# Kernel tuning notes

Measured on AMD Instinct MI355X. Metric: run time of the kernel, lower is better.

The kernel has to match this reference:

```python
import jax, jax.numpy as jnp
import numpy as np

HIDDEN = 1024
HEAD_DIM = 64
N_HEADS = HIDDEN // HEAD_DIM  # 16
BATCH = 2
SEQ = 2048
ROT_DIM = HEAD_DIM // 2  # RotaryEmbedding(head_dim // 2): only first half of head dims rotated
THETA = 10000.0
SCALE_BASE = 512.0  # lucidrains xpos default
EPS = 1e-5


def setup_inputs() -> dict:
    key = jax.random.key(0)
    ks = jax.random.split(key, 8)

    def lin(k, shape, fan_in):
        b = 1.0 / np.sqrt(fan_in)
        return jax.random.uniform(k, shape, jnp.float32, -b, b)

    return {
        "x": jax.random.normal(ks[0], (BATCH, SEQ, HIDDEN), jnp.float32),
        "ln1_w": jnp.ones((HIDDEN,), jnp.float32),
        "ln1_b": jnp.zeros((HIDDEN,), jnp.float32),
        "wqkv_w": lin(ks[1], (HIDDEN, 3 * HIDDEN), HIDDEN),
        "wg_w": lin(ks[2], (HIDDEN, HIDDEN), HIDDEN),
        "wo_w": lin(ks[3], (HIDDEN, HIDDEN), HIDDEN),
        "gn_w": jnp.ones((N_HEADS,), jnp.float32),
        "gn_b": jnp.zeros((N_HEADS,), jnp.float32),
        "ln2_w": jnp.ones((HIDDEN,), jnp.float32),
        "ln2_b": jnp.zeros((HIDDEN,), jnp.float32),
        "w1_w": lin(ks[4], (HIDDEN, HIDDEN), HIDDEN),
        "w1_b": lin(ks[5], (HIDDEN,), HIDDEN),
        "w2_w": lin(ks[6], (HIDDEN, HIDDEN), HIDDEN),
        "w2_b": lin(ks[7], (HIDDEN,), HIDDEN),
    }


def _layernorm(x, w, b):
    m = jnp.mean(x, axis=-1, keepdims=True)
    v = jnp.mean(jnp.square(x - m), axis=-1, keepdims=True)
    return (x - m) * jax.lax.rsqrt(v + EPS) * w + b


def _rotate_half(x):
    # interleaved pairs: (d r) with r=2 -> (-x2, x1)
    xs = x.reshape(x.shape[:-1] + (ROT_DIM // 2, 2))
    x1, x2 = xs[..., 0], xs[..., 1]
    return jnp.stack((-x2, x1), axis=-1).reshape(x.shape)


def _xpos_rotary(q, k):
    # lucidrains RotaryEmbedding(dim=ROT_DIM, use_xpos=True).rotate_queries_and_keys
    S = q.shape[-2]
    half = jnp.arange(0, ROT_DIM, 2, dtype=jnp.float32)
    inv_freq = 1.0 / (THETA ** (half / ROT_DIM))          # [ROT_DIM/2]
    t = jnp.arange(S, dtype=jnp.float32)
    freqs = jnp.repeat(t[:, None] * inv_freq, 2, axis=-1)  # [S, ROT_DIM] interleaved
    scale_vals = (half + 0.4 * ROT_DIM) / (1.4 * ROT_DIM)  # [ROT_DIM/2]
    power = (t - S // 2) / SCALE_BASE
    scale = scale_vals[None, :] ** power[:, None]           # [S, ROT_DIM/2]
    scale = jnp.concatenate((scale, scale), axis=-1)        # [S, ROT_DIM] (cat, not interleave)
    cos, sin = jnp.cos(freqs), jnp.sin(freqs)

    def apply(x, sc):
        xl, xr = x[..., :ROT_DIM], x[..., ROT_DIM:]
        xl = xl * cos * sc + _rotate_half(xl) * sin * sc
        return jnp.concatenate((xl, xr), axis=-1)

    return apply(q, scale), apply(k, 1.0 / scale)


def _mish(x):
    return x * jnp.tanh(jax.nn.softplus(x))


def reference(x, ln1_w, ln1_b, wqkv_w, wg_w, wo_w, gn_w, gn_b,
              ln2_w, ln2_b, w1_w, w1_b, w2_w, w2_b):
    B, S, _ = x.shape
    h = _layernorm(x, ln1_w, ln1_b)

    # qkv: [B,S,3H] -> 'B S (H D) -> B H S D' with D = 3*head_dim, then chunk 3
    qkv = (h @ wqkv_w).reshape(B, S, N_HEADS, 3 * HEAD_DIM).transpose(0, 2, 1, 3)
    q, k, v = jnp.split(qkv, 3, axis=-1)  # each [B,H,S,head_dim]
    q, k = _xpos_rotary(q, k)

    # decay mask: gamma_h^(i-j) for i>=j (causal), 0 otherwise
    gamma = 1.0 - 2.0 ** (-5.0 - jnp.arange(N_HEADS, dtype=jnp.float32))
    idx = jnp.arange(S)
    nm = (idx[:, None] - idx[None, :]).astype(jnp.float32)     # [S,S]
    decay = jnp.where(nm >= 0, gamma[:, None, None] ** nm, 0.0)  # [H,S,S]

    ret = jnp.einsum('bhsd,bhtd->bhst', q, k) * decay[None]
    ret = jnp.einsum('bhst,bhtd->bhsd', ret, v)               # [B,H,S,head_dim]

    # GroupNorm(n_heads, n_heads): normalize each head over (S, head_dim)
    m = jnp.mean(ret, axis=(2, 3), keepdims=True)
    va = jnp.mean(jnp.square(ret - m), axis=(2, 3), keepdims=True)
    ret = (ret - m) * jax.lax.rsqrt(va + EPS)
    ret = ret * gn_w[None, :, None, None] + gn_b[None, :, None, None]

    y = ret.transpose(0, 2, 1, 3).reshape(B, S, HIDDEN)       # B H S D -> B S (H D)
    y = _mish(h @ wg_w) * y
    y = y @ wo_w

    y = y + x
    z = _layernorm(y, ln2_w, ln2_b)
    ffn = jax.nn.gelu(z @ w1_w + w1_b, approximate=False) @ w2_w + w2_b
    return ffn + y
```

## Files before the change

### kernel.cpp

```cpp
#include <hip/hip_runtime.h>


constexpr int S_LEN = 2048;
constexpr int HID   = 1024;
constexpr int NH    = 16;
constexpr int HD    = 64;
constexpr int BATCH = 2;
constexpr float EPS = 1e-5f;

using short8 = __attribute__((ext_vector_type(8))) short;
using f32x4  = __attribute__((ext_vector_type(4))) float;

__device__ __forceinline__ ushort bf16rne(float x) {
  unsigned u = __float_as_uint(x);
  unsigned r = (u + 0x7fffu + ((u >> 16) & 1u)) >> 16;
  return (ushort)r;
}
__device__ __forceinline__ void split2(float x, ushort& hi, ushort& lo) {
  hi = bf16rne(x);
  float hf = __uint_as_float((unsigned)hi << 16);
  lo = bf16rne(x - hf);
}

__device__ __forceinline__ void block_reduce2(float& s, float& ss) {
  #pragma unroll
  for (int o = 32; o > 0; o >>= 1) {
    s  += __shfl_down(s, o, 64);
    ss += __shfl_down(ss, o, 64);
  }
  __shared__ float ls[4], lss[4];
  const int lane = threadIdx.x & 63;
  const int w    = threadIdx.x >> 6;
  if (lane == 0) { ls[w] = s; lss[w] = ss; }
  __syncthreads();
  if (threadIdx.x == 0) {
    float a = 0.f, b2 = 0.f;
    #pragma unroll
    for (int i = 0; i < 4; ++i) { a += ls[i]; b2 += lss[i]; }
    ls[0] = a; lss[0] = b2;
  }
  __syncthreads();
  s = ls[0]; ss = lss[0];
}

__global__ __launch_bounds__(256) void ln_split_kernel(const float* __restrict__ x,
    const float* __restrict__ w, const float* __restrict__ b,
    ushort* __restrict__ oh, ushort* __restrict__ ol) {
  const int row = blockIdx.x;
  const int t   = threadIdx.x;
  const float4 v = reinterpret_cast<const float4*>(x + (size_t)row * HID)[t];
  float s  = v.x + v.y + v.z + v.w;
  float ss = v.x*v.x + v.y*v.y + v.z*v.z + v.w*v.w;
  block_reduce2(s, ss);
  const float mean = s * (1.f / HID);
  const float var  = ss * (1.f / HID) - mean * mean;
  const float rstd = rsqrtf(var + EPS);
  const float4 wv = reinterpret_cast<const float4*>(w)[t];
  const float4 bv = reinterpret_cast<const float4*>(b)[t];
  float o[4];
  o[0] = (v.x - mean) * rstd * wv.x + bv.x;
  o[1] = (v.y - mean) * rstd * wv.y + bv.y;
  o[2] = (v.z - mean) * rstd * wv.z + bv.z;
  o[3] = (v.w - mean) * rstd * wv.w + bv.w;
  ushort4 hv, lv;
  split2(o[0], hv.x, lv.x); split2(o[1], hv.y, lv.y);
  split2(o[2], hv.z, lv.z); split2(o[3], hv.w, lv.w);
  *reinterpret_cast<ushort4*>(oh + (size_t)row * HID + t * 4) = hv;
  *reinterpret_cast<ushort4*>(ol + (size_t)row * HID + t * 4) = lv;
}

__global__ __launch_bounds__(256) void wsplit_kernel(const float* __restrict__ W,
    ushort* __restrict__ Th, ushort* __restrict__ Tl, int N) {
  __shared__ float tile[32][33];
  const int k0 = blockIdx.y * 32;
  const int n0 = blockIdx.x * 32;
  const int tx = threadIdx.x & 31, ty = threadIdx.x >> 5;
  #pragma unroll
  for (int r = 0; r < 4; ++r)
    tile[ty + 8*r][tx] = W[(size_t)(k0 + ty + 8*r) * N + n0 + tx];
  __syncthreads();
  #pragma unroll
  for (int r = 0; r < 4; ++r) {
    const int n = ty + 8*r;
    const float v = tile[tx][n];
    ushort hi, lo; split2(v, hi, lo);
    Th[(size_t)(n0 + n) * 1024 + k0 + tx] = hi;
    Tl[(size_t)(n0 + n) * 1024 + k0 + tx] = lo;
  }
}

__global__ __launch_bounds__(256) void rot_tables_kernel(float* __restrict__ tcs,
    float* __restrict__ tsn, float* __restrict__ tscq, float* __restrict__ tsck) {
  const int g = blockIdx.x * 256 + threadIdx.x;
  const int m = g & 15, s = g >> 4;
  const float invf = exp2f(-((float)(2 * m) * (1.f / 32.f)) * 13.287712379549449f);
  const float ang = (float)s * invf;
  tcs[g] = cosf(ang);
  tsn[g] = sinf(ang);
  const float p  = ((float)s - 1024.f) * (1.f / 512.f);
  const float sv = (2.f * (float)m + 12.8f) * (1.f / 44.8f);
  const float l  = log2f(sv) * p;
  tscq[g] = exp2f(l);
  tsck[g] = exp2f(-l);
}

__device__ __forceinline__ float mishf(float v) {
  return v * tanhf(log1pf(expf(v)));
}
__device__ __forceinline__ float geluf(float v) {
  return 0.5f * v * (1.f + erff(v * 0.7071067811865475f));
}

template <int EPI>
__global__ __launch_bounds__(256, 2) void gemm_mfma(
    const ushort* __restrict__ Ah, const ushort* __restrict__ Al,
    const ushort* __restrict__ Bh, const ushort* __restrict__ Bl,
    const float* __restrict__ bias, const float* __restrict__ res,
    float* __restrict__ C, ushort* __restrict__ Ch, ushort* __restrict__ Cl,
    int N, int K) {
  __shared__ ushort sA[2][128 * 64];
  __shared__ ushort sB[2][128 * 64];
  const int tid  = threadIdx.x;
  const int lane = tid & 63;
  const int w    = tid >> 6;
  const int wm   = w >> 1, wn = w & 1;
  const int rowBase = blockIdx.y * 128;
  const int colBase = blockIdx.x * 128;

  f32x4 acc[4][4] = {};

  const int l8   = lane >> 3;
  const int kswz = ((lane & 7) * 16) ^ (l8 << 4);

  for (int k0 = 0; k0 < K; k0 += 64) {
    __syncthreads();
    #pragma unroll
    for (int c = 0; c < 4; ++c) {
      const int row = w * 32 + c * 8;
      const char* gah = (const char*)(Ah + (size_t)(rowBase + row + l8) * K + k0) + kswz;
      const char* gal = (const char*)(Al + (size_t)(rowBase + row + l8) * K + k0) + kswz;
      const char* gbh = (const char*)(Bh + (size_t)(colBase + row + l8) * K + k0) + kswz;
      const char* gbl = (const char*)(Bl + (size_t)(colBase + row + l8) * K + k0) + kswz;
      __builtin_amdgcn_global_load_lds((const __attribute__((address_space(1))) void*)gah,
          (__attribute__((address_space(3))) void*)((char*)sA[0] + row * 128), 16, 0, 0);
      __builtin_amdgcn_global_load_lds((const __attribute__((address_space(1))) void*)gal,
          (__attribute__((address_space(3))) void*)((char*)sA[1] + row * 128), 16, 0, 0);
      __builtin_amdgcn_global_load_lds((const __attribute__((address_space(1))) void*)gbh,
          (__attribute__((address_space(3))) void*)((char*)sB[0] + row * 128), 16, 0, 0);
      __builtin_amdgcn_global_load_lds((const __attribute__((address_space(1))) void*)gbl,
          (__attribute__((address_space(3))) void*)((char*)sB[1] + row * 128), 16, 0, 0);
    }
    __syncthreads();
    #pragma unroll
    for (int kk = 0; kk < 2; ++kk) {
      const int kb = kk * 64 + ((lane >> 4) << 4);
      short8 ah[4], al[4], bh[4], bl[4];
      #pragma unroll
      for (int i = 0; i < 4; ++i) {
        const int row = wm * 64 + i * 16 + (lane & 15);
        const int off = row * 128 + (kb ^ ((row & 7) << 4));
        ah[i] = *(const short8*)((const char*)sA[0] + off);
        al[i] = *(const short8*)((const char*)sA[1] + off);
      }
      #pragma unroll
      for (int j = 0; j < 4; ++j) {
        const int row = wn * 64 + j * 16 + (lane & 15);
        const int off = row * 128 + (kb ^ ((row & 7) << 4));
        bh[j] = *(const short8*)((const char*)sB[0] + off);
        bl[j] = *(const short8*)((const char*)sB[1] + off);
      }
      #pragma unroll
      for (int i = 0; i < 4; ++i)
        #pragma unroll
        for (int j = 0; j < 4; ++j) {
          acc[i][j] = __builtin_amdgcn_mfma_f32_16x16x32_bf16(ah[i], bh[j], acc[i][j], 0, 0, 0);
          acc[i][j] = __builtin_amdgcn_mfma_f32_16x16x32_bf16(ah[i], bl[j], acc[i][j], 0, 0, 0);
          acc[i][j] = __builtin_amdgcn_mfma_f32_16x16x32_bf16(al[i], bh[j], acc[i][j], 0, 0, 0);
        }
    }
  }

  const int cRow = rowBase + wm * 64 + ((lane >> 4) << 2);
  const int cCol = colBase + wn * 64 + (lane & 15);
  #pragma unroll
  for (int i = 0; i < 4; ++i)
    #pragma unroll
    for (int j = 0; j < 4; ++j) {
      const int gc = cCol + j * 16;
      #pragma unroll
      for (int r = 0; r < 4; ++r) {
        const int gr = cRow + i * 16 + r;
        float v = acc[i][j][r];
        if constexpr (EPI == 1) v = mishf(v);
        if constexpr (EPI == 2) v += res[(size_t)gr * N + gc];
        if constexpr (EPI == 3) v = geluf(v + bias[gc]);
        if constexpr (EPI == 4) v += bias[gc] + res[(size_t)gr * N + gc];
        if constexpr (EPI == 3) {
          ushort hi, lo; split2(v, hi, lo);
          Ch[(size_t)gr * N + gc] = hi;
          Cl[(size_t)gr * N + gc] = lo;
        } else {
          C[(size_t)gr * N + gc] = v;
        }
      }
    }
}

__global__ __launch_bounds__(256, 2) void gemm_qkv_rot(
    const ushort* __restrict__ Ah, const ushort* __restrict__ Al,
    const ushort* __restrict__ Bh, const ushort* __restrict__ Bl,
    const float* __restrict__ tcs, const float* __restrict__ tsn,
    const float* __restrict__ tscq, const float* __restrict__ tsck,
    ushort* __restrict__ qTh, ushort* __restrict__ qTl,
    ushort* __restrict__ kTh, ushort* __restrict__ kTl,
    ushort* __restrict__ vTh, ushort* __restrict__ vTl) {
  const int N = 3072, K = 1024;
  __shared__ ushort sA[2][128 * 64];
  __shared__ ushort sB[2][128 * 64];
  const int tid  = threadIdx.x;
  const int lane = tid & 63;
  const int w    = tid >> 6;
  const int wm   = w >> 1, wn = w & 1;
  const int rowBase = blockIdx.y * 128;
  const int colBase = blockIdx.x * 128;

  f32x4 acc[4][4] = {};

  const int l8   = lane >> 3;
  const int kswz = ((lane & 7) * 16) ^ (l8 << 4);

  for (int k0 = 0; k0 < K; k0 += 64) {
    __syncthreads();
    #pragma unroll
    for (int c = 0; c < 4; ++c) {
      const int row = w * 32 + c * 8;
      const char* gah = (const char*)(Ah + (size_t)(rowBase + row + l8) * K + k0) + kswz;
      const char* gal = (const char*)(Al + (size_t)(rowBase + row + l8) * K + k0) + kswz;
      const char* gbh = (const char*)(Bh + (size_t)(colBase + row + l8) * K + k0) + kswz;
      const char* gbl = (const char*)(Bl + (size_t)(colBase + row + l8) * K + k0) + kswz;
      __builtin_amdgcn_global_load_lds((const __attribute__((address_space(1))) void*)gah,
          (__attribute__((address_space(3))) void*)((char*)sA[0] + row * 128), 16, 0, 0);
      __builtin_amdgcn_global_load_lds((const __attribute__((address_space(1))) void*)gal,
          (__attribute__((address_space(3))) void*)((char*)sA[1] + row * 128), 16, 0, 0);
      __builtin_amdgcn_global_load_lds((const __attribute__((address_space(1))) void*)gbh,
          (__attribute__((address_space(3))) void*)((char*)sB[0] + row * 128), 16, 0, 0);
      __builtin_amdgcn_global_load_lds((const __attribute__((address_space(1))) void*)gbl,
          (__attribute__((address_space(3))) void*)((char*)sB[1] + row * 128), 16, 0, 0);
    }
    __syncthreads();
    #pragma unroll
    for (int kk = 0; kk < 2; ++kk) {
      const int kb = kk * 64 + ((lane >> 4) << 4);
      short8 ah[4], al[4], bh[4], bl[4];
      #pragma unroll
      for (int i = 0; i < 4; ++i) {
        const int row = wm * 64 + i * 16 + (lane & 15);
        const int off = row * 128 + (kb ^ ((row & 7) << 4));
        ah[i] = *(const short8*)((const char*)sA[0] + off);
        al[i] = *(const short8*)((const char*)sA[1] + off);
      }
      #pragma unroll
      for (int j = 0; j < 4; ++j) {
        const int row = wn * 64 + j * 16 + (lane & 15);
        const int off = row * 128 + (kb ^ ((row & 7) << 4));
        bh[j] = *(const short8*)((const char*)sB[0] + off);
        bl[j] = *(const short8*)((const char*)sB[1] + off);
      }
      #pragma unroll
      for (int i = 0; i < 4; ++i)
        #pragma unroll
        for (int j = 0; j < 4; ++j) {
          acc[i][j] = __builtin_amdgcn_mfma_f32_16x16x32_bf16(ah[i], bh[j], acc[i][j], 0, 0, 0);
          acc[i][j] = __builtin_amdgcn_mfma_f32_16x16x32_bf16(ah[i], bl[j], acc[i][j], 0, 0, 0);
          acc[i][j] = __builtin_amdgcn_mfma_f32_16x16x32_bf16(al[i], bh[j], acc[i][j], 0, 0, 0);
        }
    }
  }

  const int c0     = colBase + wn * 64;
  const int region = (c0 >> 6) % 3;
  const int hh     = c0 / 192;
  const int cRow   = rowBase + wm * 64 + ((lane >> 4) << 2);
  const int lc     = lane & 15;

  if (region == 2) {
    #pragma unroll
    for (int j = 0; j < 4; ++j) {
      const int d = 16 * j + lc;
      #pragma unroll
      for (int i = 0; i < 4; ++i) {
        const int s0g = cRow + i * 16;
        const int bb  = s0g >> 11;
        const int s0  = s0g & 2047;
        ushort4 hv, lv;
        #pragma unroll
        for (int r = 0; r < 4; ++r) {
          ushort hi, lo; split2(acc[i][j][r], hi, lo);
          ((ushort*)&hv)[r] = hi; ((ushort*)&lv)[r] = lo;
        }
        const size_t a = ((size_t)(bb * NH + hh) * HD + d) * S_LEN + s0;
        *reinterpret_cast<ushort4*>(vTh + a) = hv;
        *reinterpret_cast<ushort4*>(vTl + a) = lv;
      }
    }
  } else {
    ushort* Oh = (region == 0) ? qTh : kTh;
    ushort* Ol = (region == 0) ? qTl : kTl;
    const float* tsc = (region == 0) ? tscq : tsck;
    #pragma unroll
    for (int j = 0; j < 4; ++j) {
      const int d  = 16 * j + lc;
      const int ii = d >> 1;
      const int im = d & 15;
      #pragma unroll
      for (int i = 0; i < 4; ++i) {
        const int s0g = cRow + i * 16;
        const int bb  = s0g >> 11;
        #pragma unroll
        for (int r = 0; r < 4; ++r) {
          const int s = (s0g + r) & 2047;
          float v = acc[i][j][r];
          float p = __shfl_xor(v, 1);
          float resv;
          if (j < 2) {
            const float cs  = tcs[s * 16 + ii];
            const float sn  = tsn[s * 16 + ii];
            const float scl = tsc[s * 16 + im];
            resv = ((lane & 1) ? (v * cs + p * sn) : (v * cs - p * sn)) * scl;
          } else {
            resv = v;
          }
          ushort hi, lo; split2(resv, hi, lo);
          const size_t a = ((size_t)(bb * NH + hh) * S_LEN + s) * HD + d;
          Oh[a] = hi; Ol[a] = lo;
        }
      }
    }
  }
}

__global__ __launch_bounds__(256, 2) void retention_mfma(
    const ushort* __restrict__ qTh, const ushort* __restrict__ qTl,
    const ushort* __restrict__ kTh, const ushort* __restrict__ kTl,
    const ushort* __restrict__ vTh, const ushort* __restrict__ vTl,
    float* __restrict__ ret) {
  const int sblk = blockIdx.x, h = blockIdx.y, b = blockIdx.z;
  const int tid = threadIdx.x, lane = tid & 63, w = tid >> 6;
  const int sBase = sblk << 6;
  const float l2g = log2f(1.f - exp2f(-5.f - (float)h));

  __shared__ ushort Qh[4096], Ql[4096], Kh[4096], Kl[4096],
                    Vh[4096], Vl[4096], Sh[4096], Sl[4096];

  const int l8   = lane >> 3;
  const int kswz = ((lane & 7) * 16) ^ (l8 << 4);

  auto stage16 = [&](const ushort* src, int pitch, ushort* dst, int r0) {
    #pragma unroll
    for (int c = 0; c < 2; ++c) {
      const int row = r0 + c * 8;
      const char* g = (const char*)(src + (size_t)(row + l8) * pitch) + kswz;
      __builtin_amdgcn_global_load_lds((const __attribute__((address_space(1))) void*)g,
          (__attribute__((address_space(3))) void*)((char*)dst + row * 128), 16, 0, 0);
    }
  };

  const size_t bh  = (size_t)(b * NH + h);
  const size_t bho = bh * (S_LEN * HD);

  stage16(qTh + bho + (size_t)sBase * HD, 64, Qh, w * 16);
  stage16(qTl + bho + (size_t)sBase * HD, 64, Ql, w * 16);

  const int sQr = (lane >> 4) << 2;
  float gs[4], gti[4];
  #pragma unroll
  for (int r = 0; r < 4; ++r) gs[r] = exp2f(l2g * (float)(w * 16 + sQr + r));
  #pragma unroll
  for (int j = 0; j < 4; ++j) gti[j] = exp2f(-l2g * (float)((lane & 15) + 16 * j));

  f32x4 acc[4] = {};

  const int aRow = w * 16 + (lane & 15);
  const int aOff = aRow * 128;
  const int aswz = (aRow & 7) << 4;

  for (int tblk = 0; tblk <= sblk; ++tblk) {
    const int tBase = tblk << 6;
    const int nmin  = sBase - tBase - 63;
    if (nmin > 0 && (float)nmin * l2g < -45.f) continue;
    __syncthreads();
    stage16(kTh + bho + (size_t)tBase * HD, 64,   Kh, w * 16);
    stage16(kTl + bho + (size_t)tBase * HD, 64,   Kl, w * 16);
    stage16(vTh + bho + tBase,              2048, Vh, w * 16);
    stage16(vTl + bho + tBase,              2048, Vl, w * 16);
    __syncthreads();

    f32x4 sc[4] = {};
    #pragma unroll
    for (int ks = 0; ks < 2; ++ks) {
      const int kb = ks * 64 + ((lane >> 4) << 4);
      const short8 qhf = *(const short8*)((const char*)Qh + aOff + (kb ^ aswz));
      const short8 qlf = *(const short8*)((const char*)Ql + aOff + (kb ^ aswz));
      #pragma unroll
      for (int j = 0; j < 4; ++j) {
        const int br = j * 16 + (lane & 15);
        const int bo = br * 128 + (kb ^ ((br & 7) << 4));
        const short8 khf = *(const short8*)((const char*)Kh + bo);
        const short8 klf = *(const short8*)((const char*)Kl + bo);
        sc[j] = __builtin_amdgcn_mfma_f32_16x16x32_bf16(qhf, khf, sc[j], 0, 0, 0);
        sc[j] = __builtin_amdgcn_mfma_f32_16x16x32_bf16(qhf, klf, sc[j], 0, 0, 0);
        sc[j] = __builtin_amdgcn_mfma_f32_16x16x32_bf16(qlf, khf, sc[j], 0, 0, 0);
      }
    }

    const float D0  = exp2f(l2g * (float)(sBase - tBase));
    const bool diag = (tBase == sBase);
    #pragma unroll
    for (int j = 0; j < 4; ++j) {
      const int tLoc  = (lane & 15) + 16 * j;
      const float gj  = D0 * gti[j];
      #pragma unroll
      for (int r = 0; r < 4; ++r) {
        const int sLoc = w * 16 + sQr + r;
        float dec = gj * gs[r];
        if (diag && sLoc < tLoc) dec = 0.f;
        const float v = sc[j][r] * dec;
        ushort hi, lo; split2(v, hi, lo);
        const int off = sLoc * 128 + ((tLoc * 2) ^ ((sLoc & 7) << 4));
        *(ushort*)((char*)Sh + off) = hi;
        *(ushort*)((char*)Sl + off) = lo;
      }
    }
    __syncthreads();

    #pragma unroll
    for (int ks = 0; ks < 2; ++ks) {
      const int kb = ks * 64 + ((lane >> 4) << 4);
      const short8 shf = *(const short8*)((const char*)Sh + aOff + (kb ^ aswz));
      const short8 slf = *(const short8*)((const char*)Sl + aOff + (kb ^ aswz));
      #pragma unroll
      for (int j = 0; j < 4; ++j) {
        const int br = j * 16 + (lane & 15);
        const int bo = br * 128 + (kb ^ ((br & 7) << 4));
        const short8 vhf = *(const short8*)((const char*)Vh + bo);
        const short8 vlf = *(const short8*)((const char*)Vl + bo);
        acc[j] = __builtin_amdgcn_mfma_f32_16x16x32_bf16(shf, vhf, acc[j], 0, 0, 0);
        acc[j] = __builtin_amdgcn_mfma_f32_16x16x32_bf16(shf, vlf, acc[j], 0, 0, 0);
        acc[j] = __builtin_amdgcn_mfma_f32_16x16x32_bf16(slf, vhf, acc[j], 0, 0, 0);
      }
    }
  }

  float* ob = ret + (bh * S_LEN + sBase) * HD;
  #pragma unroll
  for (int j = 0; j < 4; ++j)
    #pragma unroll
    for (int r = 0; r < 4; ++r)
      ob[(w * 16 + sQr + r) * 64 + j * 16 + (lane & 15)] = acc[j][r];
}

__global__ __launch_bounds__(256) void gn_kernel(const float* __restrict__ ret,
    const float* __restrict__ gm, const float* __restrict__ gn_w, const float* __restrict__ gn_b,
    ushort* __restrict__ yh, ushort* __restrict__ yl) {
  const int bh = blockIdx.x;
  const int b = bh >> 4, h = bh & 15;
  const float4* r4 = reinterpret_cast<const float4*>(ret + (size_t)bh * (S_LEN * HD));
  float s = 0.f, ss = 0.f;
  for (int i = threadIdx.x; i < S_LEN * HD / 4; i += 256) {
    const float4 v = r4[i];
    s  += v.x + v.y + v.z + v.w;
    ss += v.x*v.x + v.y*v.y + v.z*v.z + v.w*v.w;
  }
  block_reduce2(s, ss);
  const float inv  = 1.f / (float)(S_LEN * HD);
  const float mean = s * inv;
  const float var  = ss * inv - mean * mean;
  const float rstd = rsqrtf(var + EPS);
  const float a = gn_w[h] * rstd;
  const float c = gn_b[h] - mean * a;
  for (int i = threadIdx.x; i < S_LEN * HD / 4; i += 256) {
    const float4 v = r4[i];
    const int e    = i << 2;
    const int srow = e >> 6;
    const int d    = e & 63;
    const size_t oidx = (size_t)(b * S_LEN + srow) * HID + h * HD + d;
    const float4 g = *reinterpret_cast<const float4*>(gm + oidx);
    float o0 = (v.x * a + c) * g.x;
    float o1 = (v.y * a + c) * g.y;
    float o2 = (v.z * a + c) * g.z;
    float o3 = (v.w * a + c) * g.w;
    ushort4 hv, lv;
    split2(o0, hv.x, lv.x); split2(o1, hv.y, lv.y);
    split2(o2, hv.z, lv.z); split2(o3, hv.w, lv.w);
    *reinterpret_cast<ushort4*>(yh + oidx) = hv;
    *reinterpret_cast<ushort4*>(yl + oidx) = lv;
  }
}

extern "C" void kernel_launch(void* const* d_in, const int* in_sizes, int n_in,
                              void* d_out, int out_size, void* d_ws, size_t ws_size,
                              hipStream_t stream) {
  const float* x     = (const float*)d_in[0];
  const float* ln1_w = (const float*)d_in[1];
  const float* ln1_b = (const float*)d_in[2];
  const float* wqkv  = (const float*)d_in[3];
  const float* wg    = (const float*)d_in[4];
  const float* wo    = (const float*)d_in[5];
  const float* gn_w  = (const float*)d_in[6];
  const float* gn_b  = (const float*)d_in[7];
  const float* ln2_w = (const float*)d_in[8];
  const float* ln2_b = (const float*)d_in[9];
  const float* w1    = (const float*)d_in[10];
  const float* w1_b  = (const float*)d_in[11];
  const float* w2    = (const float*)d_in[12];
  const float* w2_b  = (const float*)d_in[13];

  char* ws = (char*)d_ws;
  ushort* wqkvT_h = (ushort*)(ws + 0);
  ushort* wqkvT_l = (ushort*)(ws + 6291456);
  ushort* wgT_h   = (ushort*)(ws + 12582912);
  ushort* wgT_l   = (ushort*)(ws + 14680064);
  ushort* woT_h   = (ushort*)(ws + 16777216);
  ushort* woT_l   = (ushort*)(ws + 18874368);
  ushort* w1T_h   = (ushort*)(ws + 20971520);
  ushort* w1T_l   = (ushort*)(ws + 23068672);
  ushort* w2T_h   = (ushort*)(ws + 25165824);
  ushort* w2T_l   = (ushort*)(ws + 27262976);
  ushort* h_hi    = (ushort*)(ws + 29360128);
  ushort* h_lo    = (ushort*)(ws + 37748736);
  float*  tcs     = (float*) (ws + 46137344);
  float*  tsn     = (float*) (ws + 46268416);
  float*  tscq    = (float*) (ws + 46399488);
  float*  tsck    = (float*) (ws + 46530560);
  ushort* qT_h    = (ushort*)(ws + 46661632);
  ushort* qT_l    = (ushort*)(ws + 55050240);
  ushort* kT_h    = (ushort*)(ws + 63438848);
  ushort* kT_l    = (ushort*)(ws + 71827456);
  ushort* vT_h    = (ushort*)(ws + 80216064);
  ushort* vT_l    = (ushort*)(ws + 88604672);
  float*  gmish   = (float*) (ws + 96993280);
  float*  ret     = (float*) (ws + 29360128);
  ushort* yin_h   = (ushort*)(ws + 46661632);
  ushort* yin_l   = (ushort*)(ws + 55050240);
  float*  y       = (float*) (ws + 63438848);
  ushort* z_h     = (ushort*)(ws + 80216064);
  ushort* z_l     = (ushort*)(ws + 88604672);
  ushort* f_h     = (ushort*)(ws + 96993280);
  ushort* f_l     = (ushort*)(ws + 105381888);
  float*  out     = (float*)d_out;

  wsplit_kernel<<<dim3(3072/32, 32), 256, 0, stream>>>(wqkv, wqkvT_h, wqkvT_l, 3072);
  wsplit_kernel<<<dim3(1024/32, 32), 256, 0, stream>>>(wg, wgT_h, wgT_l, 1024);
  wsplit_kernel<<<dim3(1024/32, 32), 256, 0, stream>>>(wo, woT_h, woT_l, 1024);
  wsplit_kernel<<<dim3(1024/32, 32), 256, 0, stream>>>(w1, w1T_h, w1T_l, 1024);
  wsplit_kernel<<<dim3(1024/32, 32), 256, 0, stream>>>(w2, w2T_h, w2T_l, 1024);
  rot_tables_kernel<<<128, 256, 0, stream>>>(tcs, tsn, tscq, tsck);

  ln_split_kernel<<<BATCH * S_LEN, 256, 0, stream>>>(x, ln1_w, ln1_b, h_hi, h_lo);
  gemm_mfma<1><<<dim3(1024/128, 4096/128), 256, 0, stream>>>(h_hi, h_lo, wgT_h, wgT_l,
      nullptr, nullptr, gmish, nullptr, nullptr, 1024, 1024);
  gemm_qkv_rot<<<dim3(3072/128, 4096/128), 256, 0, stream>>>(h_hi, h_lo, wqkvT_h, wqkvT_l,
      tcs, tsn, tscq, tsck, qT_h, qT_l, kT_h, kT_l, vT_h, vT_l);
  retention_mfma<<<dim3(S_LEN/64, NH, BATCH), 256, 0, stream>>>(qT_h, qT_l, kT_h, kT_l,
      vT_h, vT_l, ret);
  gn_kernel<<<BATCH * NH, 256, 0, stream>>>(ret, gmish, gn_w, gn_b, yin_h, yin_l);
  gemm_mfma<2><<<dim3(1024/128, 4096/128), 256, 0, stream>>>(yin_h, yin_l, woT_h, woT_l,
      nullptr, x, y, nullptr, nullptr, 1024, 1024);
  ln_split_kernel<<<BATCH * S_LEN, 256, 0, stream>>>(y, ln2_w, ln2_b, z_h, z_l);
  gemm_mfma<3><<<dim3(1024/128, 4096/128), 256, 0, stream>>>(z_h, z_l, w1T_h, w1T_l,
      w1_b, nullptr, nullptr, f_h, f_l, 1024, 1024);
  gemm_mfma<4><<<dim3(1024/128, 4096/128), 256, 0, stream>>>(f_h, f_l, w2T_h, w2T_l,
      w2_b, y, out, nullptr, nullptr, 1024, 1024);
}
```

Measured before the change: 614.5 us.

## Fuse gate GEMM into QKV GEMM and use 128x64 tiles for N=1024 GEMMs

Concatenates the gate weight after the QKV weight so one GEMM launch over N=4096 produces q/k/v with rotary and the mish-gated output. This removes a separate launch and fills the grid better. The three N=1024 GEMMs now use a 128x64 tile template, doubling block count from 256 to 512 to improve occupancy across CUs. The cost is less reuse per block and more A-tile reloads.

```diff
diff --git a/kernel.cpp b/kernel.cpp
--- a/kernel.cpp
+++ b/kernel.cpp
@@ -111,13 +111,117 @@
   return 0.5f * v * (1.f + erff(v * 0.7071067811865475f));
 }
 
-template <int EPI>
+template <int EPI, int BN>
 __global__ __launch_bounds__(256, 2) void gemm_mfma(
     const ushort* __restrict__ Ah, const ushort* __restrict__ Al,
     const ushort* __restrict__ Bh, const ushort* __restrict__ Bl,
     const float* __restrict__ bias, const float* __restrict__ res,
     float* __restrict__ C, ushort* __restrict__ Ch, ushort* __restrict__ Cl,
     int N, int K) {
+  constexpr int MI  = (BN == 128) ? 4 : 2;
+  constexpr int BCH = BN / 32;
+  __shared__ ushort sA[2][128 * 64];
+  __shared__ ushort sB[2][BN * 64];
+  const int tid  = threadIdx.x;
+  const int lane = tid & 63;
+  const int w    = tid >> 6;
+  const int wm   = (BN == 128) ? (w >> 1) : w;
+  const int wn   = (BN == 128) ? (w & 1)  : 0;
+  const int rowBase = blockIdx.y * 128;
+  const int colBase = blockIdx.x * BN;
+
+  f32x4 acc[MI][4] = {};
+
+  const int l8   = lane >> 3;
+  const int kswz = ((lane & 7) * 16) ^ (l8 << 4);
+
+  for (int k0 = 0; k0 < K; k0 += 64) {
+    __syncthreads();
+    #pragma unroll
+    for (int c = 0; c < 4; ++c) {
+      const int row = w * 32 + c * 8;
+      const char* gah = (const char*)(Ah + (size_t)(rowBase + row + l8) * K + k0) + kswz;
+      const char* gal = (const char*)(Al + (size_t)(rowBase + row + l8) * K + k0) + kswz;
+      __builtin_amdgcn_global_load_lds((const __attribute__((address_space(1))) void*)gah,
+          (__attribute__((address_space(3))) void*)((char*)sA[0] + row * 128), 16, 0, 0);
+      __builtin_amdgcn_global_load_lds((const __attribute__((address_space(1))) void*)gal,
+          (__attribute__((address_space(3))) void*)((char*)sA[1] + row * 128), 16, 0, 0);
+    }
+    #pragma unroll
+    for (int c = 0; c < BCH; ++c) {
+      const int row = w * (BN / 4) + c * 8;
+      const char* gbh = (const char*)(Bh + (size_t)(colBase + row + l8) * K + k0) + kswz;
+      const char* gbl = (const char*)(Bl + (size_t)(colBase + row + l8) * K + k0) + kswz;
+      __builtin_amdgcn_global_load_lds((const __attribute__((address_space(1))) void*)gbh,
+          (__attribute__((address_space(3))) void*)((char*)sB[0] + row * 128), 16, 0, 0);
+      __builtin_amdgcn_global_load_lds((const __attribute__((address_space(1))) void*)gbl,
+          (__attribute__((address_space(3))) void*)((char*)sB[1] + row * 128), 16, 0, 0);
+    }
+    __syncthreads();
+    #pragma unroll
+    for (int kk = 0; kk < 2; ++kk) {
+      const int kb = kk * 64 + ((lane >> 4) << 4);
+      short8 ah[MI], al[MI], bh[4], bl[4];
+      #pragma unroll
+      for (int i = 0; i < MI; ++i) {
+        const int row = wm * (16 * MI) + i * 16 + (lane & 15);
+        const int off = row * 128 + (kb ^ ((row & 7) << 4));
+        ah[i] = *(const short8*)((const char*)sA[0] + off);
+        al[i] = *(const short8*)((const char*)sA[1] + off);
+      }
+      #pragma unroll
+      for (int j = 0; j < 4; ++j) {
+        const int row = wn * 64 + j * 16 + (lane & 15);
+        const int off = row * 128 + (kb ^ ((row & 7) << 4));
+        bh[j] = *(const short8*)((const char*)sB[0] + off);
+        bl[j] = *(const short8*)((const char*)sB[1] + off);
+      }
+      #pragma unroll
+      for (int i = 0; i < MI; ++i)
+        #pragma unroll
+        for (int j = 0; j < 4; ++j) {
+          acc[i][j] = __builtin_amdgcn_mfma_f32_16x16x32_bf16(ah[i], bh[j], acc[i][j], 0, 0, 0);
+          acc[i][j] = __builtin_amdgcn_mfma_f32_16x16x32_bf16(ah[i], bl[j], acc[i][j], 0, 0, 0);
+          acc[i][j] = __builtin_amdgcn_mfma_f32_16x16x32_bf16(al[i], bh[j], acc[i][j], 0, 0, 0);
+        }
+    }
+  }
+
+  const int cRow = rowBase + wm * (16 * MI) + ((lane >> 4) << 2);
+  const int cCol = colBase + wn * 64 + (lane & 15);
+  #pragma unroll
+  for (int i = 0; i < MI; ++i)
+    #pragma unroll
+    for (int j = 0; j < 4; ++j) {
+      const int gc = cCol + j * 16;
+      #pragma unroll
+      for (int r = 0; r < 4; ++r) {
+        const int gr = cRow + i * 16 + r;
+        float v = acc[i][j][r];
+        if constexpr (EPI == 2) v += res[(size_t)gr * N + gc];
+        if constexpr (EPI == 3) v = geluf(v + bias[gc]);
+        if constexpr (EPI == 4) v += bias[gc] + res[(size_t)gr * N + gc];
+        if constexpr (EPI == 3) {
+          ushort hi, lo; split2(v, hi, lo);
+          Ch[(size_t)gr * N + gc] = hi;
+          Cl[(size_t)gr * N + gc] = lo;
+        } else {
+          C[(size_t)gr * N + gc] = v;
+        }
+      }
+    }
+}
+
+__global__ __launch_bounds__(256, 2) void gemm_qkvg_rot(
+    const ushort* __restrict__ Ah, const ushort* __restrict__ Al,
+    const ushort* __restrict__ Bh, const ushort* __restrict__ Bl,
+    const float* __restrict__ tcs, const float* __restrict__ tsn,
+    const float* __restrict__ tscq, const float* __restrict__ tsck,
+    ushort* __restrict__ qTh, ushort* __restrict__ qTl,
+    ushort* __restrict__ kTh, ushort* __restrict__ kTl,
+    ushort* __restrict__ vTh, ushort* __restrict__ vTl,
+    float* __restrict__ gmish) {
+  const int K = 1024;
   __shared__ ushort sA[2][128 * 64];
   __shared__ ushort sB[2][128 * 64];
   const int tid  = threadIdx.x;
@@ -180,108 +284,27 @@
     }
   }
 
+  const int c0   = colBase + wn * 64;
   const int cRow = rowBase + wm * 64 + ((lane >> 4) << 2);
-  const int cCol = colBase + wn * 64 + (lane & 15);
-  #pragma unroll
-  for (int i = 0; i < 4; ++i)
-    #pragma unroll
-    for (int j = 0; j < 4; ++j) {
-      const int gc = cCol + j * 16;
-      #pragma unroll
-      for (int r = 0; r < 4; ++r) {
-        const int gr = cRow + i * 16 + r;
-        float v = acc[i][j][r];
-        if constexpr (EPI == 1) v = mishf(v);
-        if constexpr (EPI == 2) v += res[(size_t)gr * N + gc];
-        if constexpr (EPI == 3) v = geluf(v + bias[gc]);
-        if constexpr (EPI == 4) v += bias[gc] + res[(size_t)gr * N + gc];
-        if constexpr (EPI == 3) {
-          ushort hi, lo; split2(v, hi, lo);
-          Ch[(size_t)gr * N + gc] = hi;
-          Cl[(size_t)gr * N + gc] = lo;
-        } else {
-          C[(size_t)gr * N + gc] = v;
+  const int lc   = lane & 15;
+
+  if (c0 >= 3072) {
+    const int gc0 = c0 - 3072;
+    #pragma unroll
+    for (int i = 0; i < 4; ++i)
+      #pragma unroll
+      for (int j = 0; j < 4; ++j) {
+        const int gc = gc0 + j * 16 + lc;
+        #pragma unroll
+        for (int r = 0; r < 4; ++r) {
+          const int gr = cRow + i * 16 + r;
+          gmish[(size_t)gr * 1024 + gc] = mishf(acc[i][j][r]);
         }
       }
-    }
-}
-
-__global__ __launch_bounds__(256, 2) void gemm_qkv_rot(
-    const ushort* __restrict__ Ah, const ushort* __restrict__ Al,
-    const ushort* __restrict__ Bh, const ushort* __restrict__ Bl,
-    const float* __restrict__ tcs, const float* __restrict__ tsn,
-    const float* __restrict__ tscq, const float* __restrict__ tsck,
-    ushort* __restrict__ qTh, ushort* __restrict__ qTl,
-    ushort* __restrict__ kTh, ushort* __restrict__ kTl,
-    ushort* __restrict__ vTh, ushort* __restrict__ vTl) {
-  const int N = 3072, K = 1024;
-  __shared__ ushort sA[2][128 * 64];
-  __shared__ ushort sB[2][128 * 64];
-  const int tid  = threadIdx.x;
-  const int lane = tid & 63;
-  const int w    = tid >> 6;
-  const int wm   = w >> 1, wn = w & 1;
-  const int rowBase = blockIdx.y * 128;
-  const int colBase = blockIdx.x * 128;
-
-  f32x4 acc[4][4] = {};
-
-  const int l8   = lane >> 3;
-  const int kswz = ((lane & 7) * 16) ^ (l8 << 4);
-
-  for (int k0 = 0; k0 < K; k0 += 64) {
-    __syncthreads();
-    #pragma unroll
-    for (int c = 0; c < 4; ++c) {
-      const int row = w * 32 + c * 8;
-      const char* gah = (const char*)(Ah + (size_t)(rowBase + row + l8) * K + k0) + kswz;
-      const char* gal = (const char*)(Al + (size_t)(rowBase + row + l8) * K + k0) + kswz;
-      const char* gbh = (const char*)(Bh + (size_t)(colBase + row + l8) * K + k0) + kswz;
-      const char* gbl = (const char*)(Bl + (size_t)(colBase + row + l8) * K + k0) + kswz;
-      __builtin_amdgcn_global_load_lds((const __attribute__((address_space(1))) void*)gah,
-          (__attribute__((address_space(3))) void*)((char*)sA[0] + row * 128), 16, 0, 0);
-      __builtin_amdgcn_global_load_lds((const __attribute__((address_space(1))) void*)gal,
-          (__attribute__((address_space(3))) void*)((char*)sA[1] + row * 128), 16, 0, 0);
-      __builtin_amdgcn_global_load_lds((const __attribute__((address_space(1))) void*)gbh,
-          (__attribute__((address_space(3))) void*)((char*)sB[0] + row * 128), 16, 0, 0);
-      __builtin_amdgcn_global_load_lds((const __attribute__((address_space(1))) void*)gbl,
-          (__attribute__((address_space(3))) void*)((char*)sB[1] + row * 128), 16, 0, 0);
-    }
-    __syncthreads();
-    #pragma unroll
-    for (int kk = 0; kk < 2; ++kk) {
-      const int kb = kk * 64 + ((lane >> 4) << 4);
-      short8 ah[4], al[4], bh[4], bl[4];
-      #pragma unroll
-      for (int i = 0; i < 4; ++i) {
-        const int row = wm * 64 + i * 16 + (lane & 15);
-        const int off = row * 128 + (kb ^ ((row & 7) << 4));
-        ah[i] = *(const short8*)((const char*)sA[0] + off);
-        al[i] = *(const short8*)((const char*)sA[1] + off);
-      }
-      #pragma unroll
-      for (int j = 0; j < 4; ++j) {
-        const int row = wn * 64 + j * 16 + (lane & 15);
-        const int off = row * 128 + (kb ^ ((row & 7) << 4));
-        bh[j] = *(const short8*)((const char*)sB[0] + off);
-        bl[j] = *(const short8*)((const char*)sB[1] + off);
-      }
-      #pragma unroll
-      for (int i = 0; i < 4; ++i)
-        #pragma unroll
-        for (int j = 0; j < 4; ++j) {
-          acc[i][j] = __builtin_amdgcn_mfma_f32_16x16x32_bf16(ah[i], bh[j], acc[i][j], 0, 0, 0);
-          acc[i][j] = __builtin_amdgcn_mfma_f32_16x16x32_bf16(ah[i], bl[j], acc[i][j], 0, 0, 0);
-          acc[i][j] = __builtin_amdgcn_mfma_f32_16x16x32_bf16(al[i], bh[j], acc[i][j], 0, 0, 0);
-        }
-    }
-  }
-
-  const int c0     = colBase + wn * 64;
+    return;
+  }
   const int region = (c0 >> 6) % 3;
   const int hh     = c0 / 192;
-  const int cRow   = rowBase + wm * 64 + ((lane >> 4) << 2);
-  const int lc     = lane & 15;
 
   if (region == 2) {
     #pragma unroll
@@ -516,10 +539,8 @@
   const float* w2_b  = (const float*)d_in[13];
 
   char* ws = (char*)d_ws;
-  ushort* wqkvT_h = (ushort*)(ws + 0);
-  ushort* wqkvT_l = (ushort*)(ws + 6291456);
-  ushort* wgT_h   = (ushort*)(ws + 12582912);
-  ushort* wgT_l   = (ushort*)(ws + 14680064);
+  ushort* wqkvgT_h = (ushort*)(ws + 0);
+  ushort* wqkvgT_l = (ushort*)(ws + 8388608);
   ushort* woT_h   = (ushort*)(ws + 16777216);
   ushort* woT_l   = (ushort*)(ws + 18874368);
   ushort* w1T_h   = (ushort*)(ws + 20971520);
@@ -549,26 +570,24 @@
   ushort* f_l     = (ushort*)(ws + 105381888);
   float*  out     = (float*)d_out;
 
-  wsplit_kernel<<<dim3(3072/32, 32), 256, 0, stream>>>(wqkv, wqkvT_h, wqkvT_l, 3072);
-  wsplit_kernel<<<dim3(1024/32, 32), 256, 0, stream>>>(wg, wgT_h, wgT_l, 1024);
+  wsplit_kernel<<<dim3(3072/32, 32), 256, 0, stream>>>(wqkv, wqkvgT_h, wqkvgT_l, 3072);
+  wsplit_kernel<<<dim3(1024/32, 32), 256, 0, stream>>>(wg, wqkvgT_h + 3072*1024, wqkvgT_l + 3072*1024, 1024);
   wsplit_kernel<<<dim3(1024/32, 32), 256, 0, stream>>>(wo, woT_h, woT_l, 1024);
   wsplit_kernel<<<dim3(1024/32, 32), 256, 0, stream>>>(w1, w1T_h, w1T_l, 1024);
   wsplit_kernel<<<dim3(1024/32, 32), 256, 0, stream>>>(w2, w2T_h, w2T_l, 1024);
   rot_tables_kernel<<<128, 256, 0, stream>>>(tcs, tsn, tscq, tsck);
 
   ln_split_kernel<<<BATCH * S_LEN, 256, 0, stream>>>(x, ln1_w, ln1_b, h_hi, h_lo);
-  gemm_mfma<1><<<dim3(1024/128, 4096/128), 256, 0, stream>>>(h_hi, h_lo, wgT_h, wgT_l,
-      nullptr, nullptr, gmish, nullptr, nullptr, 1024, 1024);
-  gemm_qkv_rot<<<dim3(3072/128, 4096/128), 256, 0, stream>>>(h_hi, h_lo, wqkvT_h, wqkvT_l,
-      tcs, tsn, tscq, tsck, qT_h, qT_l, kT_h, kT_l, vT_h, vT_l);
+  gemm_qkvg_rot<<<dim3(4096/128, 4096/128), 256, 0, stream>>>(h_hi, h_lo, wqkvgT_h, wqkvgT_l,
+      tcs, tsn, tscq, tsck, qT_h, qT_l, kT_h, kT_l, vT_h, vT_l, gmish);
   retention_mfma<<<dim3(S_LEN/64, NH, BATCH), 256, 0, stream>>>(qT_h, qT_l, kT_h, kT_l,
       vT_h, vT_l, ret);
   gn_kernel<<<BATCH * NH, 256, 0, stream>>>(ret, gmish, gn_w, gn_b, yin_h, yin_l);
-  gemm_mfma<2><<<dim3(1024/128, 4096/128), 256, 0, stream>>>(yin_h, yin_l, woT_h, woT_l,
+  gemm_mfma<2, 64><<<dim3(1024/64, 4096/128), 256, 0, stream>>>(yin_h, yin_l, woT_h, woT_l,
       nullptr, x, y, nullptr, nullptr, 1024, 1024);
   ln_split_kernel<<<BATCH * S_LEN, 256, 0, stream>>>(y, ln2_w, ln2_b, z_h, z_l);
-  gemm_mfma<3><<<dim3(1024/128, 4096/128), 256, 0, stream>>>(z_h, z_l, w1T_h, w1T_l,
+  gemm_mfma<3, 64><<<dim3(1024/64, 4096/128), 256, 0, stream>>>(z_h, z_l, w1T_h, w1T_l,
       w1_b, nullptr, nullptr, f_h, f_l, 1024, 1024);
-  gemm_mfma<4><<<dim3(1024/128, 4096/128), 256, 0, stream>>>(f_h, f_l, w2T_h, w2T_l,
+  gemm_mfma<4, 64><<<dim3(1024/64, 4096/128), 256, 0, stream>>>(f_h, f_l, w2T_h, w2T_l,
       w2_b, y, out, nullptr, nullptr, 1024, 1024);
 }
```

Result: faster. 582.0 us (-5.3%).
